# Kernel tuning notes

Hardware: AMD Instinct MI355X
Metric: run time of the kernel (lower is better)

The kernel has to match this reference:

```python
import jax, jax.numpy as jnp
import numpy as np

# TFMBSLinear forward: quantize input and weight to ternary {-1,0,1} via sign,
# compute out = sign(x) @ sign(W)^T (what the ternary fabric T-GEMV kernel
# computes, with zero-skip), then add float bias. The base-3 byte packing is a
# transport encoding only; the math is the ternary matmul.

def setup_inputs() -> dict:
    key = jax.random.key(0)
    k1, k2, k3 = jax.random.split(key, 3)
    B, IN, OUT = 8192, 2048, 2048
    x = jax.random.normal(k1, (B, IN), dtype=jnp.float32)
    # kaiming-uniform-ish init; only sign matters for the fabric kernel
    weight = jax.random.normal(k2, (OUT, IN), dtype=jnp.float32)
    fan_in_bound = 1.0 / np.sqrt(IN)
    bias = jax.random.uniform(k3, (OUT,), dtype=jnp.float32,
                              minval=-fan_in_bound, maxval=fan_in_bound)
    return {"input": x, "weight": weight, "bias": bias}

def reference(input, weight, bias):
    x_t = jnp.sign(input)    # ternary activations [B, IN]
    w_t = jnp.sign(weight)   # ternary weights     [OUT, IN]
    out = jnp.einsum('bi,oi->bo', x_t, w_t)  # T-GEMV accumulation, fp32
    return out + bias
```

## Files before the change

kernel.cpp:

```cpp
#include <hip/hip_runtime.h>


typedef int   intx4    __attribute__((ext_vector_type(4)));
typedef int   intx8    __attribute__((ext_vector_type(8)));
typedef float floatx16 __attribute__((ext_vector_type(16)));

static constexpr int M = 8192;
static constexpr int N = 2048;
static constexpr int K = 2048;
static constexpr int KB = K / 2;
static constexpr int BM = 128, BN = 128;

__device__ __forceinline__ unsigned nib(float v) {
    unsigned u = __float_as_uint(v);
    return (v != 0.0f) ? (0x2u | ((u >> 28) & 0x8u)) : 0u;
}

__device__ __forceinline__ unsigned pack8(const float4& a, const float4& b) {
    return  nib(a.x)        | (nib(a.y) << 4)  | (nib(a.z) << 8)  | (nib(a.w) << 12)
         | (nib(b.x) << 16) | (nib(b.y) << 20) | (nib(b.z) << 24) | (nib(b.w) << 28);
}

__global__ __launch_bounds__(256) void quant_tile(
    const float* __restrict__ x, const float* __restrict__ w,
    uint4* __restrict__ qx, uint4* __restrict__ qw, int nx, int ntot)
{
    int g = blockIdx.x * 256 + threadIdx.x;
    if (g >= ntot) return;
    const float* src; uint4* dst; int gg;
    if (g < nx) { gg = g; src = x; dst = qx; }
    else        { gg = g - nx; src = w; dst = qw; }
    const int r = gg & 31, h = (gg >> 5) & 1, c = (gg >> 6) & 31, s = gg >> 11;
    const int m = s * 32 + r;
    const float4* p = (const float4*)(src + (size_t)m * K + (c * 2 + h) * 32);
    uint4 o;
    o.x = pack8(p[0], p[1]);
    o.y = pack8(p[2], p[3]);
    o.z = pack8(p[4], p[5]);
    o.w = pack8(p[6], p[7]);
    dst[gg] = o;
}

__device__ __forceinline__ intx8 ext4(intx4 v) {
    return __builtin_shufflevector(v, v, 0, 1, 2, 3, -1, -1, -1, -1);
}

__global__ __launch_bounds__(256, 3) void tgemm_fp4(
    const char* __restrict__ A,
    const char* __restrict__ B,
    const float* __restrict__ bias,
    float* __restrict__ C)
{
    __shared__ char sA[16384];
    __shared__ char sB[16384];

    const int tid  = threadIdx.x;
    const int wave = tid >> 6;
    const int lane = tid & 63;
    const int l32  = lane & 31;
    const int half = lane >> 5;

    const int bm = blockIdx.x * BM;
    const int bn = blockIdx.y * BN;

    const char* gA = A + ((size_t)(bm >> 5) + wave) * 32768 + lane * 16;
    const char* gB = B + ((size_t)(bn >> 5) + wave) * 32768 + lane * 16;
    char* lA = sA + wave * 4096;
    char* lB = sB + wave * 4096;

    const int wm = (wave & 1) * 64;
    const int wn = (wave >> 1) * 64;

    const int aoff = (wm >> 5) * 4096 + lane * 16;
    const int boff = (wn >> 5) * 4096 + lane * 16;

    floatx16 acc[2][2] = {};

    for (int it = 0; it < 8; ++it) {
        const char* ga = gA + it * 4096;
        const char* gb = gB + it * 4096;
        #pragma unroll
        for (int t = 0; t < 4; ++t) {
            __builtin_amdgcn_global_load_lds(
                (const __attribute__((address_space(1))) void*)(ga + t * 1024),
                (__attribute__((address_space(3))) void*)(lA + t * 1024), 16, 0, 0);
            __builtin_amdgcn_global_load_lds(
                (const __attribute__((address_space(1))) void*)(gb + t * 1024),
                (__attribute__((address_space(3))) void*)(lB + t * 1024), 16, 0, 0);
        }
        __syncthreads();

        #pragma unroll
        for (int t = 0; t < 4; ++t) {
            intx4 a0 = *reinterpret_cast<const intx4*>(&sA[aoff          + t * 1024]);
            intx4 a1 = *reinterpret_cast<const intx4*>(&sA[aoff + 4096   + t * 1024]);
            intx4 b0 = *reinterpret_cast<const intx4*>(&sB[boff          + t * 1024]);
            intx4 b1 = *reinterpret_cast<const intx4*>(&sB[boff + 4096   + t * 1024]);
            acc[0][0] = __builtin_amdgcn_mfma_scale_f32_32x32x64_f8f6f4(
                ext4(a0), ext4(b0), acc[0][0], 4, 4, 0, 127, 0, 127);
            acc[0][1] = __builtin_amdgcn_mfma_scale_f32_32x32x64_f8f6f4(
                ext4(a0), ext4(b1), acc[0][1], 4, 4, 0, 127, 0, 127);
            acc[1][0] = __builtin_amdgcn_mfma_scale_f32_32x32x64_f8f6f4(
                ext4(a1), ext4(b0), acc[1][0], 4, 4, 0, 127, 0, 127);
            acc[1][1] = __builtin_amdgcn_mfma_scale_f32_32x32x64_f8f6f4(
                ext4(a1), ext4(b1), acc[1][1], 4, 4, 0, 127, 0, 127);
        }
        __syncthreads();
    }

    const int cn0 = bn + wn + l32;
    const float bc0 = bias[cn0];
    const float bc1 = bias[cn0 + 32];
    const int rbase = bm + wm + 4 * half;

    #pragma unroll
    for (int i = 0; i < 2; ++i) {
        #pragma unroll
        for (int r = 0; r < 16; ++r) {
            const int row = rbase + 32 * i + (r & 3) + 8 * (r >> 2);
            C[(size_t)row * N + cn0]      = acc[i][0][r] + bc0;
            C[(size_t)row * N + cn0 + 32] = acc[i][1][r] + bc1;
        }
    }
}

extern "C" void kernel_launch(void* const* d_in, const int* in_sizes, int n_in,
                              void* d_out, int out_size, void* d_ws, size_t ws_size,
                              hipStream_t stream) {
    const float* x    = (const float*)d_in[0];
    const float* w    = (const float*)d_in[1];
    const float* bias = (const float*)d_in[2];
    float* out = (float*)d_out;

    char* qx = (char*)d_ws;
    char* qw = qx + (size_t)M * KB;

    const int nx   = (M * KB) / 16;
    const int ntot = nx + (N * KB) / 16;
    quant_tile<<<ntot / 256, 256, 0, stream>>>(
        x, w, (uint4*)qx, (uint4*)qw, nx, ntot);

    dim3 grid(M / BM, N / BN);
    tgemm_fp4<<<grid, 256, 0, stream>>>(qx, qw, bias, out);
}
```

Baseline: 144.9 us.

## Use 256x256 tiles with 8 waves, double-buffered LDS pipeline and swizzled block order

Enlarges the GEMM tile to 256x256 with 512 threads and 4x2 MFMA accumulators per wave, so each byte staged in LDS is reused more. The K loop now double-buffers global-to-LDS loads with explicit vmcnt waits and barriers, so loads for the next step overlap the MFMAs on the current one, and uses setprio around the MFMAs. It also remaps the block index to group tiles for L2 locality. The cost is 128KB of LDS per block and more accumulator registers, which limits occupancy to about two blocks per CU, and the hand-placed waitcnt/barrier choreography is fragile.

```diff
diff --git a/kernel.cpp b/kernel.cpp
--- a/kernel.cpp
+++ b/kernel.cpp
@@ -9,7 +9,7 @@
 static constexpr int N = 2048;
 static constexpr int K = 2048;
 static constexpr int KB = K / 2;
-static constexpr int BM = 128, BN = 128;
+static constexpr int BM = 256, BN = 256;
 
 __device__ __forceinline__ unsigned nib(float v) {
     unsigned u = __float_as_uint(v);
@@ -45,76 +45,111 @@
     return __builtin_shufflevector(v, v, 0, 1, 2, 3, -1, -1, -1, -1);
 }
 
-__global__ __launch_bounds__(256, 3) void tgemm_fp4(
+#define MFMA_(A_, B_, C_) __builtin_amdgcn_mfma_scale_f32_32x32x64_f8f6f4( \
+    ext4(A_), ext4(B_), C_, 4, 4, 0, 127, 0, 127)
+
+#define GLDS(g_, l_) __builtin_amdgcn_global_load_lds(                      \
+    (const __attribute__((address_space(1))) void*)(g_),                    \
+    (__attribute__((address_space(3))) void*)(l_), 16, 0, 0)
+
+#define MFMA8()                               \
+    acc[0][0] = MFMA_(a0, b0, acc[0][0]);     \
+    acc[0][1] = MFMA_(a0, b1, acc[0][1]);     \
+    acc[1][0] = MFMA_(a1, b0, acc[1][0]);     \
+    acc[1][1] = MFMA_(a1, b1, acc[1][1]);     \
+    acc[2][0] = MFMA_(a2, b0, acc[2][0]);     \
+    acc[2][1] = MFMA_(a2, b1, acc[2][1]);     \
+    acc[3][0] = MFMA_(a3, b0, acc[3][0]);     \
+    acc[3][1] = MFMA_(a3, b1, acc[3][1])
+
+#define FRAGS(FO)                                         \
+    intx4 a0 = *(const intx4*)(fA + (FO));                \
+    intx4 a1 = *(const intx4*)(fA + (FO) + 4096);         \
+    intx4 a2 = *(const intx4*)(fA + (FO) + 8192);         \
+    intx4 a3 = *(const intx4*)(fA + (FO) + 12288);        \
+    intx4 b0 = *(const intx4*)(fB + (FO));                \
+    intx4 b1 = *(const intx4*)(fB + (FO) + 4096)
+
+__global__ __launch_bounds__(512, 2) void tgemm_fp4_256(
     const char* __restrict__ A,
     const char* __restrict__ B,
     const float* __restrict__ bias,
     float* __restrict__ C)
 {
-    __shared__ char sA[16384];
-    __shared__ char sB[16384];
+    __shared__ char smem[131072];
 
     const int tid  = threadIdx.x;
     const int wave = tid >> 6;
     const int lane = tid & 63;
     const int l32  = lane & 31;
     const int half = lane >> 5;
+    const int wm2  = wave >> 2;
+    const int wn4  = wave & 3;
 
-    const int bm = blockIdx.x * BM;
-    const int bn = blockIdx.y * BN;
+    const int bi   = blockIdx.x;
+    const int slot = bi >> 3;
+    const int bm   = ((bi & 7) * 4 + (slot >> 3)) * 256;
+    const int bn   = (slot & 7) * 256;
 
     const char* gA = A + ((size_t)(bm >> 5) + wave) * 32768 + lane * 16;
     const char* gB = B + ((size_t)(bn >> 5) + wave) * 32768 + lane * 16;
-    char* lA = sA + wave * 4096;
-    char* lB = sB + wave * 4096;
+    char* stA = smem + wave * 4096;
+    char* stB = smem + 65536 + wave * 4096;
 
-    const int wm = (wave & 1) * 64;
-    const int wn = (wave >> 1) * 64;
+    const char* fA = smem + (wm2 * 4) * 4096 + lane * 16;
+    const char* fB = smem + 65536 + (wn4 * 2) * 4096 + lane * 16;
 
-    const int aoff = (wm >> 5) * 4096 + lane * 16;
-    const int boff = (wn >> 5) * 4096 + lane * 16;
+    floatx16 acc[4][2] = {};
 
-    floatx16 acc[2][2] = {};
+    #pragma unroll
+    for (int c = 0; c < 4; ++c) {
+        GLDS(gA + c * 1024, stA + c * 1024);
+        GLDS(gB + c * 1024, stB + c * 1024);
+    }
+    asm volatile("s_waitcnt vmcnt(6)" ::: "memory");
+    __builtin_amdgcn_s_barrier();
 
-    for (int it = 0; it < 8; ++it) {
-        const char* ga = gA + it * 4096;
-        const char* gb = gB + it * 4096;
+    for (int t = 0; t < 7; ++t) {
+        const int buf  = (t & 1) * 32768;
+        const int xbuf = buf ^ 32768;
+        const char* ga = gA + (size_t)(t + 1) * 4096;
+        const char* gb = gB + (size_t)(t + 1) * 4096;
         #pragma unroll
-        for (int t = 0; t < 4; ++t) {
-            __builtin_amdgcn_global_load_lds(
-                (const __attribute__((address_space(1))) void*)(ga + t * 1024),
-                (__attribute__((address_space(3))) void*)(lA + t * 1024), 16, 0, 0);
-            __builtin_amdgcn_global_load_lds(
-                (const __attribute__((address_space(1))) void*)(gb + t * 1024),
-                (__attribute__((address_space(3))) void*)(lB + t * 1024), 16, 0, 0);
+        for (int c = 0; c < 4; ++c) {
+            FRAGS(buf + c * 1024);
+            GLDS(ga + c * 1024, stA + xbuf + c * 1024);
+            GLDS(gb + c * 1024, stB + xbuf + c * 1024);
+            asm volatile("s_waitcnt vmcnt(6)" ::: "memory");
+            __builtin_amdgcn_s_barrier();
+            __builtin_amdgcn_s_setprio(1);
+            MFMA8();
+            __builtin_amdgcn_s_setprio(0);
+            __builtin_amdgcn_s_barrier();
         }
-        __syncthreads();
-
-        #pragma unroll
-        for (int t = 0; t < 4; ++t) {
-            intx4 a0 = *reinterpret_cast<const intx4*>(&sA[aoff          + t * 1024]);
-            intx4 a1 = *reinterpret_cast<const intx4*>(&sA[aoff + 4096   + t * 1024]);
-            intx4 b0 = *reinterpret_cast<const intx4*>(&sB[boff          + t * 1024]);
-            intx4 b1 = *reinterpret_cast<const intx4*>(&sB[boff + 4096   + t * 1024]);
-            acc[0][0] = __builtin_amdgcn_mfma_scale_f32_32x32x64_f8f6f4(
-                ext4(a0), ext4(b0), acc[0][0], 4, 4, 0, 127, 0, 127);
-            acc[0][1] = __builtin_amdgcn_mfma_scale_f32_32x32x64_f8f6f4(
-                ext4(a0), ext4(b1), acc[0][1], 4, 4, 0, 127, 0, 127);
-            acc[1][0] = __builtin_amdgcn_mfma_scale_f32_32x32x64_f8f6f4(
-                ext4(a1), ext4(b0), acc[1][0], 4, 4, 0, 127, 0, 127);
-            acc[1][1] = __builtin_amdgcn_mfma_scale_f32_32x32x64_f8f6f4(
-                ext4(a1), ext4(b1), acc[1][1], 4, 4, 0, 127, 0, 127);
-        }
-        __syncthreads();
     }
 
-    const int cn0 = bn + wn + l32;
+    {
+        const int buf = 32768;
+        #pragma unroll
+        for (int c = 0; c < 4; ++c) {
+            FRAGS(buf + c * 1024);
+            if (c == 0) { asm volatile("s_waitcnt vmcnt(4)" ::: "memory"); __builtin_amdgcn_s_barrier(); }
+            if (c == 1) { asm volatile("s_waitcnt vmcnt(2)" ::: "memory"); __builtin_amdgcn_s_barrier(); }
+            if (c == 2) { asm volatile("s_waitcnt vmcnt(0)" ::: "memory"); __builtin_amdgcn_s_barrier(); }
+            __builtin_amdgcn_s_setprio(1);
+            MFMA8();
+            __builtin_amdgcn_s_setprio(0);
+            if (c < 3) __builtin_amdgcn_s_barrier();
+        }
+    }
+
+    const int cn0 = bn + wn4 * 64 + l32;
     const float bc0 = bias[cn0];
     const float bc1 = bias[cn0 + 32];
-    const int rbase = bm + wm + 4 * half;
+    const int rbase = bm + wm2 * 128 + 4 * half;
 
     #pragma unroll
-    for (int i = 0; i < 2; ++i) {
+    for (int i = 0; i < 4; ++i) {
         #pragma unroll
         for (int r = 0; r < 16; ++r) {
             const int row = rbase + 32 * i + (r & 3) + 8 * (r >> 2);
@@ -140,6 +175,6 @@
     quant_tile<<<ntot / 256, 256, 0, stream>>>(
         x, w, (uint4*)qx, (uint4*)qw, nx, ntot);
 
-    dim3 grid(M / BM, N / BN);
-    tgemm_fp4<<<grid, 256, 0, stream>>>(qx, qw, bias, out);
+    tgemm_fp4_256<<<dim3((M / BM) * (N / BN)), dim3(512), 0, stream>>>(
+        qx, qw, bias, out);
 }
```

Result: no change. 142.6 us (-1.6%).
